# Performance work log

Measured on AMD Instinct MI355X. Metric: run time of the kernel, lower is better.

## Reference

```python
import jax, jax.numpy as jnp
import numpy as np

MAX_MARKER = 16


def setup_inputs() -> dict:
    key = jax.random.key(0)
    ks = jax.random.split(key, 7)
    B, W, H = 65536, 512, 8
    s1 = 1.0 / np.sqrt(W)
    s2 = 1.0 / np.sqrt(H)
    return {
        "x": jax.random.normal(ks[0], (B, W), dtype=jnp.float32),
        "W1": jax.random.uniform(ks[1], (H, W), jnp.float32, -s1, s1),
        "b1": jax.random.uniform(ks[2], (H,), jnp.float32, -s1, s1),
        "W2": jax.random.uniform(ks[3], (H, H), jnp.float32, -s2, s2),
        "b2": jax.random.uniform(ks[4], (H,), jnp.float32, -s2, s2),
        "W3": jax.random.uniform(ks[5], (W, H), jnp.float32, -s2, s2),
        "b3": jax.random.uniform(ks[6], (W,), jnp.float32, -s2, s2),
    }


def reference(x, W1, b1, W2, b2, W3, b3):
    # tiny MLP: window -> 8 -> 8 -> window
    h = jax.nn.relu(x @ W1.T + b1)
    h = jax.nn.relu(h @ W2.T + b2)
    y = h @ W3.T + b3
    p = jax.nn.softmax(y, axis=1)
    # force endpoints on (x.data[:,0]=1; x.data[:,-1]=1)
    p = p.at[:, 0].set(1.0).at[:, -1].set(1.0)
    # top-k along dim 1; threshold = min of the top-k values per row
    top_vals, _ = jax.lax.top_k(p, MAX_MARKER)
    thr = top_vals[:, -1:]  # sorted desc -> last is min, shape [B,1]
    # binary mask writes: >= thr -> 1, else 0
    return jnp.where(p >= thr, 1.0, 0.0).astype(p.dtype)
```

## Files before the change

### kernel.cpp

```cpp
#include <hip/hip_runtime.h>
#include <math.h>

#define B_ROWS 65536
#define WDIM 512
#define HDIM 8
#define THREADS 512

typedef float native_float4 __attribute__((ext_vector_type(4)));

template<int CTRL, int ROWM>
__device__ __forceinline__ float dpp_mov(float oldv, float x) {
    return __int_as_float(__builtin_amdgcn_update_dpp(
        __float_as_int(oldv), __float_as_int(x), CTRL, ROWM, 0xF, false));
}

__device__ __forceinline__ float wave_sum(float x) {
    x += dpp_mov<0x121, 0xF>(0.f, x);
    x += dpp_mov<0x122, 0xF>(0.f, x);
    x += dpp_mov<0x124, 0xF>(0.f, x);
    x += dpp_mov<0x128, 0xF>(0.f, x);
    x += dpp_mov<0x142, 0xA>(0.f, x);
    x += dpp_mov<0x143, 0xC>(0.f, x);
    return __int_as_float(__builtin_amdgcn_readlane(__float_as_int(x), 63));
}

__device__ __forceinline__ float wave_max(float x) {
    x = fmaxf(x, dpp_mov<0x121, 0xF>(-INFINITY, x));
    x = fmaxf(x, dpp_mov<0x122, 0xF>(-INFINITY, x));
    x = fmaxf(x, dpp_mov<0x124, 0xF>(-INFINITY, x));
    x = fmaxf(x, dpp_mov<0x128, 0xF>(-INFINITY, x));
    x = fmaxf(x, dpp_mov<0x142, 0xA>(-INFINITY, x));
    x = fmaxf(x, dpp_mov<0x143, 0xC>(-INFINITY, x));
    return __int_as_float(__builtin_amdgcn_readlane(__float_as_int(x), 63));
}

__device__ __forceinline__ float dot8(native_float4 a0, native_float4 a1,
                                      native_float4 b0, native_float4 b1) {
    float s = a0.x * b0.x;
    s = fmaf(a0.y, b0.y, s); s = fmaf(a0.z, b0.z, s); s = fmaf(a0.w, b0.w, s);
    s = fmaf(a1.x, b1.x, s); s = fmaf(a1.y, b1.y, s);
    s = fmaf(a1.z, b1.z, s); s = fmaf(a1.w, b1.w, s);
    return s;
}

__global__ __launch_bounds__(THREADS, 4)
void fused_mlp_topk(const float* __restrict__ x,
                    const float* __restrict__ W1,
                    const float* __restrict__ b1,
                    const float* __restrict__ W2,
                    const float* __restrict__ b2,
                    const float* __restrict__ W3,
                    const float* __restrict__ b3,
                    float* __restrict__ out)
{
    __shared__ __align__(16) float sW1[HDIM * WDIM];
    __shared__ __align__(16) float sW3t[HDIM * WDIM];
    __shared__ __align__(16) float sb3[WDIM];

    const int tid = threadIdx.x;
    for (int i = tid; i < HDIM * WDIM; i += THREADS) sW1[i] = W1[i];
    for (int i = tid; i < HDIM * WDIM; i += THREADS) {
        int r = i >> 3, k = i & 7;
        sW3t[k * WDIM + r] = W3[i];
    }
    for (int i = tid; i < WDIM; i += THREADS) sb3[i] = b3[i];
    __syncthreads();

    const int lane = tid & 63;
    const int wave_id = blockIdx.x * (THREADS / 64) + (tid >> 6);

    const native_float4* sW1v = reinterpret_cast<const native_float4*>(sW1);
    const native_float4* sW3v = reinterpret_cast<const native_float4*>(sW3t);
    const native_float4* sb3v = reinterpret_cast<const native_float4*>(sb3);

    int ra = wave_id;

    #pragma unroll 1
    for (int it = 0; it < 8; ++it) {
        const native_float4* xp = reinterpret_cast<const native_float4*>(x + (size_t)ra * WDIM);
        native_float4 x0 = __builtin_nontemporal_load(xp + lane);
        native_float4 x1 = __builtin_nontemporal_load(xp + lane + 64);

        float pa[HDIM];
        #pragma unroll
        for (int j = 0; j < HDIM; ++j) {
            native_float4 w0 = sW1v[j * 128 + lane];
            native_float4 w1 = sW1v[j * 128 + lane + 64];
            pa[j] = dot8(x0, x1, w0, w1);
        }
        float h1[HDIM];
        #pragma unroll
        for (int j = 0; j < HDIM; ++j) {
            float sa = wave_sum(pa[j]) + b1[j];
            h1[j] = sa > 0.f ? sa : 0.f;
        }

        float h2[HDIM];
        #pragma unroll
        for (int j = 0; j < HDIM; ++j) {
            float va = b2[j];
            #pragma unroll
            for (int k = 0; k < HDIM; ++k) {
                const float w = W2[j * HDIM + k];
                va = fmaf(w, h1[k], va);
            }
            h2[j] = va > 0.f ? va : 0.f;
        }

        native_float4 y0 = sb3v[lane];
        native_float4 y1 = sb3v[lane + 64];
        #pragma unroll
        for (int k = 0; k < HDIM; ++k) {
            const float ha = h2[k];
            native_float4 w0 = sW3v[k * 128 + lane];
            native_float4 w1 = sW3v[k * 128 + lane + 64];
            y0.x = fmaf(ha, w0.x, y0.x); y0.y = fmaf(ha, w0.y, y0.y);
            y0.z = fmaf(ha, w0.z, y0.z); y0.w = fmaf(ha, w0.w, y0.w);
            y1.x = fmaf(ha, w1.x, y1.x); y1.y = fmaf(ha, w1.y, y1.y);
            y1.z = fmaf(ha, w1.z, y1.z); y1.w = fmaf(ha, w1.w, y1.w);
        }

        float lma = fmaxf(fmaxf(fmaxf(y0.x, y0.y), fmaxf(y0.z, y0.w)),
                          fmaxf(fmaxf(y1.x, y1.y), fmaxf(y1.z, y1.w)));
        float ma = wave_max(lma);

        float p[8];
        p[0] = expf(y0.x - ma); p[1] = expf(y0.y - ma);
        p[2] = expf(y0.z - ma); p[3] = expf(y0.w - ma);
        p[4] = expf(y1.x - ma); p[5] = expf(y1.y - ma);
        p[6] = expf(y1.z - ma); p[7] = expf(y1.w - ma);
        float lsa = ((p[0] + p[1]) + (p[2] + p[3])) + ((p[4] + p[5]) + (p[6] + p[7]));
        float sa = wave_sum(lsa);

        #pragma unroll
        for (int t = 0; t < 8; ++t) p[t] = p[t] / sa;
        if (lane == 0)  p[0] = 1.0f;
        if (lane == 63) p[7] = 1.0f;

        unsigned Ua = 0x30000000u;
        for (int b = 27; b >= 0; --b) {
            const unsigned bit = 1u << b;
            const float cfa = __uint_as_float(Ua | bit);
            int ca = 0;
            #pragma unroll
            for (int t = 0; t < 8; ++t)
                ca += __popcll(__ballot(p[t] > cfa));
            if (ca >= 16) Ua |= bit;
        }
        const float thra = __uint_as_float(Ua + 1u);

        native_float4 r0, r1;
        r0.x = p[0] >= thra ? 1.f : 0.f;  r0.y = p[1] >= thra ? 1.f : 0.f;
        r0.z = p[2] >= thra ? 1.f : 0.f;  r0.w = p[3] >= thra ? 1.f : 0.f;
        r1.x = p[4] >= thra ? 1.f : 0.f;  r1.y = p[5] >= thra ? 1.f : 0.f;
        r1.z = p[6] >= thra ? 1.f : 0.f;  r1.w = p[7] >= thra ? 1.f : 0.f;

        native_float4* oa = reinterpret_cast<native_float4*>(out + (size_t)ra * WDIM);
        __builtin_nontemporal_store(r0, oa + lane);
        __builtin_nontemporal_store(r1, oa + lane + 64);

        ra += 8192;
    }
}

extern "C" void kernel_launch(void* const* d_in, const int* in_sizes, int n_in,
                              void* d_out, int out_size, void* d_ws, size_t ws_size,
                              hipStream_t stream) {
    const float* x  = (const float*)d_in[0];
    const float* W1 = (const float*)d_in[1];
    const float* b1 = (const float*)d_in[2];
    const float* W2 = (const float*)d_in[3];
    const float* b2 = (const float*)d_in[4];
    const float* W3 = (const float*)d_in[5];
    const float* b3 = (const float*)d_in[6];
    float* out = (float*)d_out;

    fused_mlp_topk<<<dim3(1024), dim3(THREADS), 0, stream>>>(x, W1, b1, W2, b2, W3, b3, out);
}
```

Measured before the change: 402.7 us.

## Prefetch next row of x and run top-k on unnormalized exponentials

The load of the next row's x is issued early, during the current row's softmax and top-k work, so global memory latency overlaps compute. Softmax normalization (the sum reduction and divisions) is dropped because top-k ordering does not depend on it. The two forced endpoints are handled outside the radix search, which now looks for 14 other elements, and those endpoints are set to 1 in the output. The launch-bounds occupancy hint is lowered from 4 to 3, giving the compiler more registers to hold the prefetched values, at the risk of fewer resident waves.

After: 384.2 us. 4.6% less time.

```diff
diff --git a/kernel.cpp b/kernel.cpp
--- a/kernel.cpp
+++ b/kernel.cpp
@@ -43,7 +43,7 @@
     return s;
 }
 
-__global__ __launch_bounds__(THREADS, 4)
+__global__ __launch_bounds__(THREADS, 3)
 void fused_mlp_topk(const float* __restrict__ x,
                     const float* __restrict__ W1,
                     const float* __restrict__ b1,
@@ -74,13 +74,12 @@
     const native_float4* sb3v = reinterpret_cast<const native_float4*>(sb3);
 
     int ra = wave_id;
+    const native_float4* xp = reinterpret_cast<const native_float4*>(x + (size_t)ra * WDIM);
+    native_float4 x0 = __builtin_nontemporal_load(xp + lane);
+    native_float4 x1 = __builtin_nontemporal_load(xp + lane + 64);
 
     #pragma unroll 1
     for (int it = 0; it < 8; ++it) {
-        const native_float4* xp = reinterpret_cast<const native_float4*>(x + (size_t)ra * WDIM);
-        native_float4 x0 = __builtin_nontemporal_load(xp + lane);
-        native_float4 x1 = __builtin_nontemporal_load(xp + lane + 64);
-
         float pa[HDIM];
         #pragma unroll
         for (int j = 0; j < HDIM; ++j) {
@@ -114,28 +113,29 @@
             const float ha = h2[k];
             native_float4 w0 = sW3v[k * 128 + lane];
             native_float4 w1 = sW3v[k * 128 + lane + 64];
-            y0.x = fmaf(ha, w0.x, y0.x); y0.y = fmaf(ha, w0.y, y0.y);
-            y0.z = fmaf(ha, w0.z, y0.z); y0.w = fmaf(ha, w0.w, y0.w);
-            y1.x = fmaf(ha, w1.x, y1.x); y1.y = fmaf(ha, w1.y, y1.y);
-            y1.z = fmaf(ha, w1.z, y1.z); y1.w = fmaf(ha, w1.w, y1.w);
+            y0 += ha * w0;  y1 += ha * w1;
+        }
+
+        const int nra = ra + 8192;
+        native_float4 nx0, nx1;
+        if (it < 7) {
+            const native_float4* nxp = reinterpret_cast<const native_float4*>(x + (size_t)nra * WDIM);
+            nx0 = __builtin_nontemporal_load(nxp + lane);
+            nx1 = __builtin_nontemporal_load(nxp + lane + 64);
         }
 
         float lma = fmaxf(fmaxf(fmaxf(y0.x, y0.y), fmaxf(y0.z, y0.w)),
                           fmaxf(fmaxf(y1.x, y1.y), fmaxf(y1.z, y1.w)));
         float ma = wave_max(lma);
 
-        float p[8];
-        p[0] = expf(y0.x - ma); p[1] = expf(y0.y - ma);
-        p[2] = expf(y0.z - ma); p[3] = expf(y0.w - ma);
-        p[4] = expf(y1.x - ma); p[5] = expf(y1.y - ma);
-        p[6] = expf(y1.z - ma); p[7] = expf(y1.w - ma);
-        float lsa = ((p[0] + p[1]) + (p[2] + p[3])) + ((p[4] + p[5]) + (p[6] + p[7]));
-        float sa = wave_sum(lsa);
+        float ea[8];
+        ea[0] = expf(y0.x - ma); ea[1] = expf(y0.y - ma);
+        ea[2] = expf(y0.z - ma); ea[3] = expf(y0.w - ma);
+        ea[4] = expf(y1.x - ma); ea[5] = expf(y1.y - ma);
+        ea[6] = expf(y1.z - ma); ea[7] = expf(y1.w - ma);
 
-        #pragma unroll
-        for (int t = 0; t < 8; ++t) p[t] = p[t] / sa;
-        if (lane == 0)  p[0] = 1.0f;
-        if (lane == 63) p[7] = 1.0f;
+        if (lane == 0)  ea[0] = 0.f;
+        if (lane == 63) ea[7] = 0.f;
 
         unsigned Ua = 0x30000000u;
         for (int b = 27; b >= 0; --b) {
@@ -144,22 +144,25 @@
             int ca = 0;
             #pragma unroll
             for (int t = 0; t < 8; ++t)
-                ca += __popcll(__ballot(p[t] > cfa));
-            if (ca >= 16) Ua |= bit;
+                ca += __popcll(__ballot(ea[t] > cfa));
+            if (ca >= 14) Ua |= bit;
         }
         const float thra = __uint_as_float(Ua + 1u);
 
         native_float4 r0, r1;
-        r0.x = p[0] >= thra ? 1.f : 0.f;  r0.y = p[1] >= thra ? 1.f : 0.f;
-        r0.z = p[2] >= thra ? 1.f : 0.f;  r0.w = p[3] >= thra ? 1.f : 0.f;
-        r1.x = p[4] >= thra ? 1.f : 0.f;  r1.y = p[5] >= thra ? 1.f : 0.f;
-        r1.z = p[6] >= thra ? 1.f : 0.f;  r1.w = p[7] >= thra ? 1.f : 0.f;
+        r0.x = ea[0] >= thra ? 1.f : 0.f;  r0.y = ea[1] >= thra ? 1.f : 0.f;
+        r0.z = ea[2] >= thra ? 1.f : 0.f;  r0.w = ea[3] >= thra ? 1.f : 0.f;
+        r1.x = ea[4] >= thra ? 1.f : 0.f;  r1.y = ea[5] >= thra ? 1.f : 0.f;
+        r1.z = ea[6] >= thra ? 1.f : 0.f;  r1.w = ea[7] >= thra ? 1.f : 0.f;
+        if (lane == 0)  r0.x = 1.f;
+        if (lane == 63) r1.w = 1.f;
 
         native_float4* oa = reinterpret_cast<native_float4*>(out + (size_t)ra * WDIM);
         __builtin_nontemporal_store(r0, oa + lane);
         __builtin_nontemporal_store(r1, oa + lane + 64);
 
-        ra += 8192;
+        ra = nra;
+        x0 = nx0; x1 = nx1;
     }
 }
 
```
